# Kernel optimization log

Measured on AMD Instinct MI355X. Metric: run time of the kernel, lower is better.

Reference implementation:

```python
import jax, jax.numpy as jnp
import numpy as np

N = 100000
IN_CH = 256
OUT_CH = 64
HID = 2 * OUT_CH


def _gcn_norm(edge_index, num_nodes):
    # add self-loops, compute symmetric normalization (PyG GCNConv default)
    loop = jnp.arange(num_nodes, dtype=edge_index.dtype)
    row = jnp.concatenate([edge_index[0], loop])  # source
    col = jnp.concatenate([edge_index[1], loop])  # target
    deg = jax.ops.segment_sum(jnp.ones_like(col, dtype=jnp.float32), col,
                              num_segments=num_nodes)
    dinv = jnp.where(deg > 0, jax.lax.rsqrt(deg), 0.0)
    norm = dinv[row] * dinv[col]  # [E+N]
    return row, col, norm


def _gcn_conv(x, W, b, row, col, norm, num_nodes):
    h = x @ W  # [N, F_out] linear first (F_out <= F_in here)
    msg = norm[:, None] * h[row]  # gather + scale, [E+N, F_out]
    out = jax.ops.segment_sum(msg, col, num_segments=num_nodes)
    return out + b


def setup_inputs() -> dict:
    key = jax.random.key(0)
    k1, k2, k3, k4 = jax.random.split(key, 4)
    x = jax.random.normal(k1, (N, IN_CH), dtype=jnp.float32)
    edge_index = jax.random.randint(k2, (2, 1600000), 0, N, dtype=jnp.int64)
    # Glorot-style init like PyG
    W1 = jax.random.normal(k3, (IN_CH, HID), dtype=jnp.float32) / np.sqrt(IN_CH)
    W2 = jax.random.normal(k4, (HID, OUT_CH), dtype=jnp.float32) / np.sqrt(HID)
    b1 = jnp.zeros((HID,), dtype=jnp.float32)
    b2 = jnp.zeros((OUT_CH,), dtype=jnp.float32)
    return {"x": x, "edge_index": edge_index, "W1": W1, "b1": b1, "W2": W2, "b2": b2}


def reference(x, edge_index, W1, b1, W2, b2):
    row, col, norm = _gcn_norm(edge_index, N)
    h = _gcn_conv(x, W1, b1, row, col, norm, N)
    h = jax.nn.relu(h)
    return _gcn_conv(h, W2, b2, row, col, norm, N)
```

## Files before the change

### kernel.cpp

```cpp
#include <hip/hip_runtime.h>
#include <hip/hip_bf16.h>
#include <math.h>

#define IN_CH 256
#define HID 128
#define OUT_CH 64
#define MAXB 128
#define CAP 18432
#define TILE 8192

typedef __attribute__((ext_vector_type(8))) short bf16x8;
typedef __attribute__((ext_vector_type(4))) float f32x4;

__device__ __forceinline__ unsigned int pack_bf2(float a, float b) {
    __hip_bfloat162 h = __float22bfloat162_rn(make_float2(a, b));
    return *(unsigned int*)&h;
}
__device__ __forceinline__ float2 bf2_to_f2(unsigned int v) {
    float2 r;
    r.x = __uint_as_float(v << 16);
    r.y = __uint_as_float(v & 0xffff0000u);
    return r;
}
__device__ __forceinline__ unsigned short f_to_bf1(float f) {
    __hip_bfloat16 h = __float2bfloat16(f);
    return *(unsigned short*)&h;
}
__device__ __forceinline__ void acc8(float4& a, float4& b, uint4 w) {
    float2 p0 = bf2_to_f2(w.x), p1 = bf2_to_f2(w.y);
    float2 p2 = bf2_to_f2(w.z), p3 = bf2_to_f2(w.w);
    a.x += p0.x; a.y += p0.y; a.z += p1.x; a.w += p1.y;
    b.x += p2.x; b.y += p2.y; b.z += p3.x; b.w += p3.y;
}
__device__ __forceinline__ void acc4(float4& a, uint2 w) {
    float2 p0 = bf2_to_f2(w.x), p1 = bf2_to_f2(w.y);
    a.x += p0.x; a.y += p0.y; a.z += p1.x; a.w += p1.y;
}

__global__ void detect_kernel(const void* ei, int E, int N, int* flag) {
    const long long* p = (const long long*)ei;
    int ok = 1;
    for (int j = 0; j < 16; ++j) {
        long long v = p[j];
        if (v < 0 || v >= (long long)N) { ok = 0; break; }
    }
    *flag = ok;
}

__device__ __forceinline__ int edge_at(const void* ei, long long pos, bool is64) {
    return is64 ? (int)((const long long*)ei)[pos] : ((const int*)ei)[pos];
}

__global__ __launch_bounds__(256) void wprep_kernel(const float* __restrict__ W1,
                                                    const float* __restrict__ W2,
                                                    unsigned short* __restrict__ wT1,
                                                    unsigned short* __restrict__ wT2) {
    int t = blockIdx.x * 256 + threadIdx.x;
    if (t < IN_CH * HID) {
        int k = t >> 7, n = t & 127;
        wT1[n * IN_CH + k] = f_to_bf1(W1[t]);
    }
    if (t < HID * OUT_CH) {
        int k = t >> 6, n = t & 63;
        wT2[n * HID + k] = f_to_bf1(W2[t]);
    }
}

__global__ __launch_bounds__(256) void bucket_kernel(const void* ei, int E, int B,
                                                     const int* __restrict__ flag,
                                                     unsigned int* __restrict__ recs,
                                                     int* __restrict__ bcur) {
    __shared__ int cnt[MAXB], off[MAXB], cur[MAXB], gb[MAXB];
    __shared__ unsigned int staged[TILE];
    const bool is64 = (*flag != 0);
    const int t = threadIdx.x;
    const long long base = (long long)blockIdx.x * TILE;

    for (int b = t; b < MAXB; b += 256) cnt[b] = 0;
    __syncthreads();

    for (int i = t; i < TILE; i += 256) {
        long long e = base + i;
        if (e < E) {
            int c = edge_at(ei, (long long)E + e, is64);
            atomicAdd(&cnt[c >> 10], 1);
        }
    }
    __syncthreads();

    if (t < MAXB) off[t] = cnt[t];
    __syncthreads();
    for (int o = 1; o < MAXB; o <<= 1) {
        int v = 0;
        if (t < MAXB && t >= o) v = off[t - o];
        __syncthreads();
        if (t < MAXB) off[t] += v;
        __syncthreads();
    }
    if (t < MAXB) {
        int ex = off[t] - cnt[t];
        off[t] = ex;
        cur[t] = ex;
        gb[t] = 0;
        if (t < B && cnt[t] > 0) gb[t] = atomicAdd(&bcur[t], cnt[t]);
    }
    __syncthreads();

    for (int i = t; i < TILE; i += 256) {
        long long e = base + i;
        if (e < E) {
            int r = edge_at(ei, e, is64);
            int c = edge_at(ei, (long long)E + e, is64);
            int b = c >> 10;
            int p = atomicAdd(&cur[b], 1);
            staged[p] = ((unsigned int)r << 10) | (unsigned int)(c & 1023);
        }
    }
    __syncthreads();

    int wv = t >> 6, ln = t & 63;
    for (int b = wv; b < B; b += 4) {
        int s = off[b];
        int n = cnt[b];
        int gbase = gb[b];
        if (gbase + n > CAP) n = (CAP > gbase) ? (CAP - gbase) : 0;
        for (int j = ln; j < n; j += 64)
            recs[(size_t)b * CAP + gbase + j] = staged[s + j];
    }
}

__global__ __launch_bounds__(512) void csr_kernel(unsigned int* __restrict__ recs,
                                                  const int* __restrict__ bcur,
                                                  int* __restrict__ starts,
                                                  int* __restrict__ cnts,
                                                  float* __restrict__ dinv, int N) {
    __shared__ int degs[1024], lcur[1024], part[512];
    __shared__ unsigned int rows[CAP];
    const int b = blockIdx.x, t = threadIdx.x;
    const int n = min(bcur[b], CAP);
    const size_t rb = (size_t)b * CAP;

    degs[t] = 0;
    degs[t + 512] = 0;
    __syncthreads();
    for (int i = t; i < n; i += 512)
        atomicAdd(&degs[recs[rb + i] & 1023], 1);
    __syncthreads();

    int s0 = degs[2 * t], s1 = degs[2 * t + 1];
    part[t] = s0 + s1;
    __syncthreads();
    for (int o = 1; o < 512; o <<= 1) {
        int v = (t >= o) ? part[t - o] : 0;
        __syncthreads();
        part[t] += v;
        __syncthreads();
    }
    int ex = part[t] - (s0 + s1);
    lcur[2 * t] = ex;
    lcur[2 * t + 1] = ex + s0;

    int node = (b << 10) + 2 * t;
    if (node < N) {
        starts[node] = b * CAP + ex;
        cnts[node] = s0;
        dinv[node] = rsqrtf((float)(s0 + 1));
    }
    if (node + 1 < N) {
        starts[node + 1] = b * CAP + ex + s0;
        cnts[node + 1] = s1;
        dinv[node + 1] = rsqrtf((float)(s1 + 1));
    }
    __syncthreads();

    for (int i = t; i < n; i += 512) {
        unsigned int rc = recs[rb + i];
        int p = atomicAdd(&lcur[rc & 1023], 1);
        rows[p] = rc >> 10;
    }
    __syncthreads();
    for (int i = t; i < n; i += 512) recs[rb + i] = rows[i];
}

__global__ __launch_bounds__(256) void gemm1_kernel(const float* __restrict__ x,
                                                    const unsigned short* __restrict__ wT,
                                                    const float* __restrict__ dinv,
                                                    unsigned short* __restrict__ u, int N) {
    __shared__ uint4 lds4[2048];
    unsigned char* lds = (unsigned char*)lds4;
    const int t = threadIdx.x;
    const int bm0 = blockIdx.x * 128;
    const int wid = t >> 6, lane = t & 63;
    const int l16 = lane & 15, lq = lane >> 4;

    f32x4 acc[2][8];
#pragma unroll
    for (int mf = 0; mf < 2; ++mf)
#pragma unroll
        for (int nf = 0; nf < 8; ++nf) acc[mf][nf] = (f32x4){0.f, 0.f, 0.f, 0.f};

    for (int kc = 0; kc < IN_CH; kc += 64) {
#pragma unroll
        for (int it = 0; it < 4; ++it) {
            int uu = it * 256 + t;
            int r = uu >> 3, c8 = uu & 7;
            int row = bm0 + r;
            float4 v0 = make_float4(0.f, 0.f, 0.f, 0.f), v1 = v0;
            if (row < N) {
                const float* p = &x[(long long)row * IN_CH + kc + c8 * 8];
                v0 = *(const float4*)p;
                v1 = *(const float4*)(p + 4);
            }
            uint4 w;
            w.x = pack_bf2(v0.x, v0.y);
            w.y = pack_bf2(v0.z, v0.w);
            w.z = pack_bf2(v1.x, v1.y);
            w.w = pack_bf2(v1.z, v1.w);
            int off = (r * 128 + c8 * 16) ^ ((r & 7) << 4);
            *(uint4*)&lds[off] = w;
        }
#pragma unroll
        for (int it = 0; it < 4; ++it) {
            int uu = it * 256 + t;
            int n = uu >> 3, c8 = uu & 7;
            uint4 w = *(const uint4*)&wT[n * IN_CH + kc + c8 * 8];
            int off = 16384 + ((n * 128 + c8 * 16) ^ ((n & 7) << 4));
            *(uint4*)&lds[off] = w;
        }
        __syncthreads();
#pragma unroll
        for (int kk = 0; kk < 2; ++kk) {
            int kbyte = kk * 64 + lq * 16;
            bf16x8 a[2], b[8];
#pragma unroll
            for (int mf = 0; mf < 2; ++mf) {
                int r = wid * 32 + mf * 16 + l16;
                int off = (r * 128 + kbyte) ^ ((r & 7) << 4);
                a[mf] = *(const bf16x8*)&lds[off];
            }
#pragma unroll
            for (int nf = 0; nf < 8; ++nf) {
                int n = nf * 16 + l16;
                int off = 16384 + ((n * 128 + kbyte) ^ ((n & 7) << 4));
                b[nf] = *(const bf16x8*)&lds[off];
            }
#pragma unroll
            for (int mf = 0; mf < 2; ++mf)
#pragma unroll
                for (int nf = 0; nf < 8; ++nf)
                    acc[mf][nf] = __builtin_amdgcn_mfma_f32_16x16x32_bf16(
                        a[mf], b[nf], acc[mf][nf], 0, 0, 0);
        }
        __syncthreads();
    }
#pragma unroll
    for (int mf = 0; mf < 2; ++mf) {
#pragma unroll
        for (int j = 0; j < 4; ++j) {
            int row = bm0 + wid * 32 + mf * 16 + lq * 4 + j;
            if (row < N) {
                float dv = dinv[row];
#pragma unroll
                for (int nf = 0; nf < 8; ++nf)
                    u[(long long)row * HID + nf * 16 + l16] = f_to_bf1(acc[mf][nf][j] * dv);
            }
        }
    }
}

__global__ __launch_bounds__(256) void gemm2_kernel(const unsigned short* __restrict__ A,
                                                    const unsigned short* __restrict__ wT,
                                                    const float* __restrict__ dinv,
                                                    unsigned short* __restrict__ u, int N) {
    __shared__ uint4 lds4[1536];
    unsigned char* lds = (unsigned char*)lds4;
    const int t = threadIdx.x;
    const int bm0 = blockIdx.x * 128;
    const int wid = t >> 6, lane = t & 63;
    const int l16 = lane & 15, lq = lane >> 4;

    f32x4 acc[2][4];
#pragma unroll
    for (int mf = 0; mf < 2; ++mf)
#pragma unroll
        for (int nf = 0; nf < 4; ++nf) acc[mf][nf] = (f32x4){0.f, 0.f, 0.f, 0.f};

    for (int kc = 0; kc < HID; kc += 64) {
#pragma unroll
        for (int it = 0; it < 4; ++it) {
            int uu = it * 256 + t;
            int r = uu >> 3, c8 = uu & 7;
            int row = bm0 + r;
            uint4 w = make_uint4(0, 0, 0, 0);
            if (row < N) w = *(const uint4*)&A[(long long)row * HID + kc + c8 * 8];
            int off = (r * 128 + c8 * 16) ^ ((r & 7) << 4);
            *(uint4*)&lds[off] = w;
        }
#pragma unroll
        for (int it = 0; it < 2; ++it) {
            int uu = it * 256 + t;
            int n = uu >> 3, c8 = uu & 7;
            uint4 w = *(const uint4*)&wT[n * HID + kc + c8 * 8];
            int off = 16384 + ((n * 128 + c8 * 16) ^ ((n & 7) << 4));
            *(uint4*)&lds[off] = w;
        }
        __syncthreads();
#pragma unroll
        for (int kk = 0; kk < 2; ++kk) {
            int kbyte = kk * 64 + lq * 16;
            bf16x8 a[2], b[4];
#pragma unroll
            for (int mf = 0; mf < 2; ++mf) {
                int r = wid * 32 + mf * 16 + l16;
                int off = (r * 128 + kbyte) ^ ((r & 7) << 4);
                a[mf] = *(const bf16x8*)&lds[off];
            }
#pragma unroll
            for (int nf = 0; nf < 4; ++nf) {
                int n = nf * 16 + l16;
                int off = 16384 + ((n * 128 + kbyte) ^ ((n & 7) << 4));
                b[nf] = *(const bf16x8*)&lds[off];
            }
#pragma unroll
            for (int mf = 0; mf < 2; ++mf)
#pragma unroll
                for (int nf = 0; nf < 4; ++nf)
                    acc[mf][nf] = __builtin_amdgcn_mfma_f32_16x16x32_bf16(
                        a[mf], b[nf], acc[mf][nf], 0, 0, 0);
        }
        __syncthreads();
    }
#pragma unroll
    for (int mf = 0; mf < 2; ++mf) {
#pragma unroll
        for (int j = 0; j < 4; ++j) {
            int row = bm0 + wid * 32 + mf * 16 + lq * 4 + j;
            if (row < N) {
                float dv = dinv[row];
#pragma unroll
                for (int nf = 0; nf < 4; ++nf)
                    u[(long long)row * OUT_CH + nf * 16 + l16] = f_to_bf1(acc[mf][nf][j] * dv);
            }
        }
    }
}

__global__ __launch_bounds__(256) void agg1_kernel(const uint4* __restrict__ u,
                                                   const int* __restrict__ starts,
                                                   const int* __restrict__ cnts,
                                                   const unsigned int* __restrict__ srow,
                                                   const float* __restrict__ dinv,
                                                   const float* __restrict__ bias,
                                                   unsigned short* __restrict__ out, int N) {
    int wave = threadIdx.x >> 6;
    int lane = threadIdx.x & 63;
    int q = lane >> 4, l16 = lane & 15;
    int node = blockIdx.x * 16 + wave * 4 + q;
    bool act = node < N;
    int nd = act ? node : N - 1;

    float4 sa = make_float4(0.f, 0.f, 0.f, 0.f), sb = sa;
    acc8(sa, sb, u[(size_t)nd * 16 + l16]);

    int beg = starts[nd];
    int cnt = act ? cnts[nd] : 0;
    int j = 0;
    for (; j + 7 < cnt; j += 8) {
        uint4 g[8];
#pragma unroll
        for (int k = 0; k < 8; ++k)
            g[k] = u[(size_t)(int)srow[beg + j + k] * 16 + l16];
#pragma unroll
        for (int k = 0; k < 8; ++k) acc8(sa, sb, g[k]);
    }
    if (j + 3 < cnt) {
        uint4 g[4];
#pragma unroll
        for (int k = 0; k < 4; ++k)
            g[k] = u[(size_t)(int)srow[beg + j + k] * 16 + l16];
#pragma unroll
        for (int k = 0; k < 4; ++k) acc8(sa, sb, g[k]);
        j += 4;
    }
    for (; j < cnt; ++j)
        acc8(sa, sb, u[(size_t)(int)srow[beg + j] * 16 + l16]);

    if (act) {
        float dv = dinv[nd];
        float4 b0 = *(const float4*)&bias[l16 * 8];
        float4 b1v = *(const float4*)&bias[l16 * 8 + 4];
        float o0 = fmaxf(fmaf(dv, sa.x, b0.x), 0.f);
        float o1 = fmaxf(fmaf(dv, sa.y, b0.y), 0.f);
        float o2 = fmaxf(fmaf(dv, sa.z, b0.z), 0.f);
        float o3 = fmaxf(fmaf(dv, sa.w, b0.w), 0.f);
        float o4 = fmaxf(fmaf(dv, sb.x, b1v.x), 0.f);
        float o5 = fmaxf(fmaf(dv, sb.y, b1v.y), 0.f);
        float o6 = fmaxf(fmaf(dv, sb.z, b1v.z), 0.f);
        float o7 = fmaxf(fmaf(dv, sb.w, b1v.w), 0.f);
        uint4 w;
        w.x = pack_bf2(o0, o1);
        w.y = pack_bf2(o2, o3);
        w.z = pack_bf2(o4, o5);
        w.w = pack_bf2(o6, o7);
        *(uint4*)&out[(size_t)node * HID + l16 * 8] = w;
    }
}

__global__ __launch_bounds__(256) void agg2_kernel(const uint2* __restrict__ u,
                                                   const int* __restrict__ starts,
                                                   const int* __restrict__ cnts,
                                                   const unsigned int* __restrict__ srow,
                                                   const float* __restrict__ dinv,
                                                   const float* __restrict__ bias,
                                                   float* __restrict__ out, int N) {
    int wave = threadIdx.x >> 6;
    int lane = threadIdx.x & 63;
    int q = lane >> 4, l16 = lane & 15;
    int node = blockIdx.x * 16 + wave * 4 + q;
    bool act = node < N;
    int nd = act ? node : N - 1;

    float4 s = make_float4(0.f, 0.f, 0.f, 0.f);
    acc4(s, u[(size_t)nd * 16 + l16]);

    int beg = starts[nd];
    int cnt = act ? cnts[nd] : 0;
    int j = 0;
    for (; j + 7 < cnt; j += 8) {
        uint2 g[8];
#pragma unroll
        for (int k = 0; k < 8; ++k)
            g[k] = u[(size_t)(int)srow[beg + j + k] * 16 + l16];
#pragma unroll
        for (int k = 0; k < 8; ++k) acc4(s, g[k]);
    }
    if (j + 3 < cnt) {
        uint2 g[4];
#pragma unroll
        for (int k = 0; k < 4; ++k)
            g[k] = u[(size_t)(int)srow[beg + j + k] * 16 + l16];
#pragma unroll
        for (int k = 0; k < 4; ++k) acc4(s, g[k]);
        j += 4;
    }
    for (; j < cnt; ++j)
        acc4(s, u[(size_t)(int)srow[beg + j] * 16 + l16]);

    if (act) {
        float dv = dinv[nd];
        float4 bb = *(const float4*)&bias[l16 * 4];
        float4 o;
        o.x = fmaf(dv, s.x, bb.x);
        o.y = fmaf(dv, s.y, bb.y);
        o.z = fmaf(dv, s.z, bb.z);
        o.w = fmaf(dv, s.w, bb.w);
        *(float4*)&out[(size_t)node * OUT_CH + l16 * 4] = o;
    }
}

extern "C" void kernel_launch(void* const* d_in, const int* in_sizes, int n_in,
                              void* d_out, int out_size, void* d_ws, size_t ws_size,
                              hipStream_t stream) {
    const float* x  = (const float*)d_in[0];
    const void*  ei = d_in[1];
    const float* W1 = (const float*)d_in[2];
    const float* b1 = (const float*)d_in[3];
    const float* W2 = (const float*)d_in[4];
    const float* b2 = (const float*)d_in[5];
    float* out = (float*)d_out;

    const int N = in_sizes[0] / IN_CH;
    const int E = in_sizes[1] / 2;
    const int B = (N + 1023) >> 10;

    char* ws = (char*)d_ws;
    size_t off = 0;
    auto alloc = [&](size_t bytes) -> void* {
        void* p = ws + off;
        off += (bytes + 255) & ~(size_t)255;
        return p;
    };
    int*            flag   = (int*)alloc(256);
    int*            bcur   = (int*)alloc(MAXB * 4);
    int*            starts = (int*)alloc((size_t)N * 4);
    int*            cnts   = (int*)alloc((size_t)N * 4);
    float*          dinv   = (float*)alloc((size_t)N * 4);
    unsigned int*   recs   = (unsigned int*)alloc((size_t)B * CAP * 4);
    unsigned short* wT1    = (unsigned short*)alloc((size_t)IN_CH * HID * 2);
    unsigned short* wT2    = (unsigned short*)alloc((size_t)HID * OUT_CH * 2);
    unsigned short* u1     = (unsigned short*)alloc((size_t)N * HID * 2);
    unsigned short* hagg   = (unsigned short*)alloc((size_t)N * HID * 2);
    unsigned short* u2     = (unsigned short*)alloc((size_t)N * OUT_CH * 2);

    (void)hipMemsetAsync(bcur, 0, MAXB * 4, stream);
    detect_kernel<<<1, 1, 0, stream>>>(ei, E, N, flag);
    wprep_kernel<<<128, 256, 0, stream>>>(W1, W2, wT1, wT2);
    int tblocks = (E + TILE - 1) / TILE;
    bucket_kernel<<<tblocks, 256, 0, stream>>>(ei, E, B, flag, recs, bcur);
    csr_kernel<<<B, 512, 0, stream>>>(recs, bcur, starts, cnts, dinv, N);

    int gblocks = (N + 127) / 128;
    int ablocks = (N + 15) / 16;
    gemm1_kernel<<<gblocks, 256, 0, stream>>>(x, wT1, dinv, u1, N);
    agg1_kernel<<<ablocks, 256, 0, stream>>>((const uint4*)u1, starts, cnts, recs,
                                             dinv, b1, hagg, N);
    gemm2_kernel<<<gblocks, 256, 0, stream>>>(hagg, wT2, dinv, u2, N);
    agg2_kernel<<<ablocks, 256, 0, stream>>>((const uint2*)u2, starts, cnts, recs,
                                             dinv, b2, out, N);
}
```

Before: 199.7 us.

## Coarsely sort CSR neighbor lists by source block for gather locality

The CSR build now counts edges per (target, source-block) pair, with 16 source ranges of 8192 nodes, in a 64KB shared histogram. It scans that histogram and scatters row ids straight to a new global array, so each node's neighbors are grouped by source range. This replaces the shared-memory staging buffer and copy-back. The aim is better cache locality for the feature gathers in the aggregation kernels, at the cost of more LDS per block, extra serial scan work per thread, and an extra workspace buffer.

```diff
diff --git a/kernel.cpp b/kernel.cpp
--- a/kernel.cpp
+++ b/kernel.cpp
@@ -8,6 +8,8 @@
 #define MAXB 128
 #define CAP 18432
 #define TILE 8192
+#define NBLK 16
+#define SRCSH 13
 
 typedef __attribute__((ext_vector_type(8))) short bf16x8;
 typedef __attribute__((ext_vector_type(4))) float f32x4;
@@ -129,25 +131,33 @@
     }
 }
 
-__global__ __launch_bounds__(512) void csr_kernel(unsigned int* __restrict__ recs,
+__global__ __launch_bounds__(512) void csr_kernel(const unsigned int* __restrict__ recs,
                                                   const int* __restrict__ bcur,
+                                                  unsigned int* __restrict__ srowS,
                                                   int* __restrict__ starts,
                                                   int* __restrict__ cnts,
                                                   float* __restrict__ dinv, int N) {
-    __shared__ int degs[1024], lcur[1024], part[512];
-    __shared__ unsigned int rows[CAP];
+    __shared__ unsigned int cnt2[1024 * NBLK];
+    __shared__ int part[512];
     const int b = blockIdx.x, t = threadIdx.x;
     const int n = min(bcur[b], CAP);
     const size_t rb = (size_t)b * CAP;
 
-    degs[t] = 0;
-    degs[t + 512] = 0;
-    __syncthreads();
-    for (int i = t; i < n; i += 512)
-        atomicAdd(&degs[recs[rb + i] & 1023], 1);
-    __syncthreads();
-
-    int s0 = degs[2 * t], s1 = degs[2 * t + 1];
+    for (int i = t; i < 1024 * NBLK; i += 512) cnt2[i] = 0;
+    __syncthreads();
+
+    for (int i = t; i < n; i += 512) {
+        unsigned int rc = recs[rb + i];
+        atomicAdd(&cnt2[(rc & 1023) * NBLK + (rc >> (10 + SRCSH))], 1u);
+    }
+    __syncthreads();
+
+    const int base_e = t * 32;
+    int s0 = 0, s1 = 0;
+#pragma unroll
+    for (int k = 0; k < NBLK; ++k) s0 += (int)cnt2[base_e + k];
+#pragma unroll
+    for (int k = 0; k < NBLK; ++k) s1 += (int)cnt2[base_e + NBLK + k];
     part[t] = s0 + s1;
     __syncthreads();
     for (int o = 1; o < 512; o <<= 1) {
@@ -157,9 +167,15 @@
         __syncthreads();
     }
     int ex = part[t] - (s0 + s1);
-    lcur[2 * t] = ex;
-    lcur[2 * t + 1] = ex + s0;
-
+    {
+        unsigned int run = (unsigned int)ex;
+#pragma unroll
+        for (int k = 0; k < 32; ++k) {
+            unsigned int c = cnt2[base_e + k];
+            cnt2[base_e + k] = run;
+            run += c;
+        }
+    }
     int node = (b << 10) + 2 * t;
     if (node < N) {
         starts[node] = b * CAP + ex;
@@ -175,11 +191,9 @@
 
     for (int i = t; i < n; i += 512) {
         unsigned int rc = recs[rb + i];
-        int p = atomicAdd(&lcur[rc & 1023], 1);
-        rows[p] = rc >> 10;
-    }
-    __syncthreads();
-    for (int i = t; i < n; i += 512) recs[rb + i] = rows[i];
+        unsigned int p = atomicAdd(&cnt2[(rc & 1023) * NBLK + (rc >> (10 + SRCSH))], 1u);
+        srowS[rb + p] = rc >> 10;
+    }
 }
 
 __global__ __launch_bounds__(256) void gemm1_kernel(const float* __restrict__ x,
@@ -486,6 +500,7 @@
     int*            cnts   = (int*)alloc((size_t)N * 4);
     float*          dinv   = (float*)alloc((size_t)N * 4);
     unsigned int*   recs   = (unsigned int*)alloc((size_t)B * CAP * 4);
+    unsigned int*   srowS  = (unsigned int*)alloc((size_t)B * CAP * 4);
     unsigned short* wT1    = (unsigned short*)alloc((size_t)IN_CH * HID * 2);
     unsigned short* wT2    = (unsigned short*)alloc((size_t)HID * OUT_CH * 2);
     unsigned short* u1     = (unsigned short*)alloc((size_t)N * HID * 2);
@@ -497,14 +512,14 @@
     wprep_kernel<<<128, 256, 0, stream>>>(W1, W2, wT1, wT2);
     int tblocks = (E + TILE - 1) / TILE;
     bucket_kernel<<<tblocks, 256, 0, stream>>>(ei, E, B, flag, recs, bcur);
-    csr_kernel<<<B, 512, 0, stream>>>(recs, bcur, starts, cnts, dinv, N);
+    csr_kernel<<<B, 512, 0, stream>>>(recs, bcur, srowS, starts, cnts, dinv, N);
 
     int gblocks = (N + 127) / 128;
     int ablocks = (N + 15) / 16;
     gemm1_kernel<<<gblocks, 256, 0, stream>>>(x, wT1, dinv, u1, N);
-    agg1_kernel<<<ablocks, 256, 0, stream>>>((const uint4*)u1, starts, cnts, recs,
+    agg1_kernel<<<ablocks, 256, 0, stream>>>((const uint4*)u1, starts, cnts, srowS,
                                              dinv, b1, hagg, N);
     gemm2_kernel<<<gblocks, 256, 0, stream>>>(hagg, wT2, dinv, u2, N);
-    agg2_kernel<<<ablocks, 256, 0, stream>>>((const uint2*)u2, starts, cnts, recs,
+    agg2_kernel<<<ablocks, 256, 0, stream>>>((const uint2*)u2, starts, cnts, srowS,
                                              dinv, b2, out, N);
 }
```

New measurement: 208.4 us. +4.4%, slower.

## Store GEMM outputs in 16-column chunk-major layout and aggregate per chunk

Applied to the files above, without the earlier changes.

GEMM outputs u1, hagg and u2 are now stored in column-chunk-major order ([chunk][node][16] bf16), and the aggregation kernels use a second grid dimension so each block processes a single 16-column chunk. Each feature table slice (N*32 bytes) is small enough to stay cache-resident while edges gather random rows, which should cut the miss traffic from scattered neighbour reads. In exchange, the edge index lists are re-read once per chunk (8x and 4x), each gather moves only 4 bytes per lane, and gemm2 now reads its A operand through strided chunk addressing.

```diff
diff --git a/kernel.cpp b/kernel.cpp
--- a/kernel.cpp
+++ b/kernel.cpp
@@ -25,16 +25,6 @@
 __device__ __forceinline__ unsigned short f_to_bf1(float f) {
     __hip_bfloat16 h = __float2bfloat16(f);
     return *(unsigned short*)&h;
-}
-__device__ __forceinline__ void acc8(float4& a, float4& b, uint4 w) {
-    float2 p0 = bf2_to_f2(w.x), p1 = bf2_to_f2(w.y);
-    float2 p2 = bf2_to_f2(w.z), p3 = bf2_to_f2(w.w);
-    a.x += p0.x; a.y += p0.y; a.z += p1.x; a.w += p1.y;
-    b.x += p2.x; b.y += p2.y; b.z += p3.x; b.w += p3.y;
-}
-__device__ __forceinline__ void acc4(float4& a, uint2 w) {
-    float2 p0 = bf2_to_f2(w.x), p1 = bf2_to_f2(w.y);
-    a.x += p0.x; a.y += p0.y; a.z += p1.x; a.w += p1.y;
 }
 
 __global__ void detect_kernel(const void* ei, int E, int N, int* flag) {
@@ -262,7 +252,7 @@
                 float dv = dinv[row];
 #pragma unroll
                 for (int nf = 0; nf < 8; ++nf)
-                    u[(long long)row * HID + nf * 16 + l16] = f_to_bf1(acc[mf][nf][j] * dv);
+                    u[((size_t)nf * N + row) * 16 + l16] = f_to_bf1(acc[mf][nf][j] * dv);
             }
         }
     }
@@ -292,7 +282,11 @@
             int r = uu >> 3, c8 = uu & 7;
             int row = bm0 + r;
             uint4 w = make_uint4(0, 0, 0, 0);
-            if (row < N) w = *(const uint4*)&A[(long long)row * HID + kc + c8 * 8];
+            if (row < N) {
+                int chunk = (kc >> 4) + (c8 >> 1);
+                const unsigned short* Ac = A + (size_t)chunk * N * 16;
+                w = *(const uint4*)&Ac[(size_t)row * 16 + (c8 & 1) * 8];
+            }
             int off = (r * 128 + c8 * 16) ^ ((r & 7) << 4);
             *(uint4*)&lds[off] = w;
         }
@@ -339,122 +333,126 @@
                 float dv = dinv[row];
 #pragma unroll
                 for (int nf = 0; nf < 4; ++nf)
-                    u[(long long)row * OUT_CH + nf * 16 + l16] = f_to_bf1(acc[mf][nf][j] * dv);
-            }
-        }
-    }
-}
-
-__global__ __launch_bounds__(256) void agg1_kernel(const uint4* __restrict__ u,
+                    u[((size_t)nf * N + row) * 16 + l16] = f_to_bf1(acc[mf][nf][j] * dv);
+            }
+        }
+    }
+}
+
+__global__ __launch_bounds__(256) void agg1_kernel(const unsigned int* __restrict__ u,
                                                    const int* __restrict__ starts,
                                                    const int* __restrict__ cnts,
                                                    const unsigned int* __restrict__ srow,
                                                    const float* __restrict__ dinv,
                                                    const float* __restrict__ bias,
-                                                   unsigned short* __restrict__ out, int N) {
-    int wave = threadIdx.x >> 6;
-    int lane = threadIdx.x & 63;
-    int q = lane >> 4, l16 = lane & 15;
-    int node = blockIdx.x * 16 + wave * 4 + q;
+                                                   unsigned int* __restrict__ out, int N) {
+    const int c = blockIdx.y;
+    const int g = threadIdx.x >> 3, k = threadIdx.x & 7;
+    int node = blockIdx.x * 32 + g;
     bool act = node < N;
     int nd = act ? node : N - 1;
-
-    float4 sa = make_float4(0.f, 0.f, 0.f, 0.f), sb = sa;
-    acc8(sa, sb, u[(size_t)nd * 16 + l16]);
-
+    const unsigned int* tab = u + (size_t)c * N * 8;
+
+    float2 s = bf2_to_f2(tab[(size_t)nd * 8 + k]);
     int beg = starts[nd];
     int cnt = act ? cnts[nd] : 0;
     int j = 0;
     for (; j + 7 < cnt; j += 8) {
-        uint4 g[8];
-#pragma unroll
-        for (int k = 0; k < 8; ++k)
-            g[k] = u[(size_t)(int)srow[beg + j + k] * 16 + l16];
-#pragma unroll
-        for (int k = 0; k < 8; ++k) acc8(sa, sb, g[k]);
+        unsigned int gv[8];
+#pragma unroll
+        for (int q = 0; q < 8; ++q)
+            gv[q] = tab[(size_t)(int)srow[beg + j + q] * 8 + k];
+#pragma unroll
+        for (int q = 0; q < 8; ++q) {
+            float2 v = bf2_to_f2(gv[q]);
+            s.x += v.x;
+            s.y += v.y;
+        }
     }
     if (j + 3 < cnt) {
-        uint4 g[4];
-#pragma unroll
-        for (int k = 0; k < 4; ++k)
-            g[k] = u[(size_t)(int)srow[beg + j + k] * 16 + l16];
-#pragma unroll
-        for (int k = 0; k < 4; ++k) acc8(sa, sb, g[k]);
+        unsigned int gv[4];
+#pragma unroll
+        for (int q = 0; q < 4; ++q)
+            gv[q] = tab[(size_t)(int)srow[beg + j + q] * 8 + k];
+#pragma unroll
+        for (int q = 0; q < 4; ++q) {
+            float2 v = bf2_to_f2(gv[q]);
+            s.x += v.x;
+            s.y += v.y;
+        }
         j += 4;
     }
-    for (; j < cnt; ++j)
-        acc8(sa, sb, u[(size_t)(int)srow[beg + j] * 16 + l16]);
+    for (; j < cnt; ++j) {
+        float2 v = bf2_to_f2(tab[(size_t)(int)srow[beg + j] * 8 + k]);
+        s.x += v.x;
+        s.y += v.y;
+    }
 
     if (act) {
         float dv = dinv[nd];
-        float4 b0 = *(const float4*)&bias[l16 * 8];
-        float4 b1v = *(const float4*)&bias[l16 * 8 + 4];
-        float o0 = fmaxf(fmaf(dv, sa.x, b0.x), 0.f);
-        float o1 = fmaxf(fmaf(dv, sa.y, b0.y), 0.f);
-        float o2 = fmaxf(fmaf(dv, sa.z, b0.z), 0.f);
-        float o3 = fmaxf(fmaf(dv, sa.w, b0.w), 0.f);
-        float o4 = fmaxf(fmaf(dv, sb.x, b1v.x), 0.f);
-        float o5 = fmaxf(fmaf(dv, sb.y, b1v.y), 0.f);
-        float o6 = fmaxf(fmaf(dv, sb.z, b1v.z), 0.f);
-        float o7 = fmaxf(fmaf(dv, sb.w, b1v.w), 0.f);
-        uint4 w;
-        w.x = pack_bf2(o0, o1);
-        w.y = pack_bf2(o2, o3);
-        w.z = pack_bf2(o4, o5);
-        w.w = pack_bf2(o6, o7);
-        *(uint4*)&out[(size_t)node * HID + l16 * 8] = w;
-    }
-}
-
-__global__ __launch_bounds__(256) void agg2_kernel(const uint2* __restrict__ u,
+        float2 bb = *(const float2*)&bias[c * 16 + k * 2];
+        float ox = fmaxf(fmaf(dv, s.x, bb.x), 0.f);
+        float oy = fmaxf(fmaf(dv, s.y, bb.y), 0.f);
+        out[(size_t)c * N * 8 + (size_t)node * 8 + k] = pack_bf2(ox, oy);
+    }
+}
+
+__global__ __launch_bounds__(256) void agg2_kernel(const unsigned int* __restrict__ u,
                                                    const int* __restrict__ starts,
                                                    const int* __restrict__ cnts,
                                                    const unsigned int* __restrict__ srow,
                                                    const float* __restrict__ dinv,
                                                    const float* __restrict__ bias,
                                                    float* __restrict__ out, int N) {
-    int wave = threadIdx.x >> 6;
-    int lane = threadIdx.x & 63;
-    int q = lane >> 4, l16 = lane & 15;
-    int node = blockIdx.x * 16 + wave * 4 + q;
+    const int c = blockIdx.y;
+    const int g = threadIdx.x >> 3, k = threadIdx.x & 7;
+    int node = blockIdx.x * 32 + g;
     bool act = node < N;
     int nd = act ? node : N - 1;
-
-    float4 s = make_float4(0.f, 0.f, 0.f, 0.f);
-    acc4(s, u[(size_t)nd * 16 + l16]);
-
+    const unsigned int* tab = u + (size_t)c * N * 8;
+
+    float2 s = bf2_to_f2(tab[(size_t)nd * 8 + k]);
     int beg = starts[nd];
     int cnt = act ? cnts[nd] : 0;
     int j = 0;
     for (; j + 7 < cnt; j += 8) {
-        uint2 g[8];
-#pragma unroll
-        for (int k = 0; k < 8; ++k)
-            g[k] = u[(size_t)(int)srow[beg + j + k] * 16 + l16];
-#pragma unroll
-        for (int k = 0; k < 8; ++k) acc4(s, g[k]);
+        unsigned int gv[8];
+#pragma unroll
+        for (int q = 0; q < 8; ++q)
+            gv[q] = tab[(size_t)(int)srow[beg + j + q] * 8 + k];
+#pragma unroll
+        for (int q = 0; q < 8; ++q) {
+            float2 v = bf2_to_f2(gv[q]);
+            s.x += v.x;
+            s.y += v.y;
+        }
     }
     if (j + 3 < cnt) {
-        uint2 g[4];
-#pragma unroll
-        for (int k = 0; k < 4; ++k)
-            g[k] = u[(size_t)(int)srow[beg + j + k] * 16 + l16];
-#pragma unroll
-        for (int k = 0; k < 4; ++k) acc4(s, g[k]);
+        unsigned int gv[4];
+#pragma unroll
+        for (int q = 0; q < 4; ++q)
+            gv[q] = tab[(size_t)(int)srow[beg + j + q] * 8 + k];
+#pragma unroll
+        for (int q = 0; q < 4; ++q) {
+            float2 v = bf2_to_f2(gv[q]);
+            s.x += v.x;
+            s.y += v.y;
+        }
         j += 4;
     }
-    for (; j < cnt; ++j)
-        acc4(s, u[(size_t)(int)srow[beg + j] * 16 + l16]);
+    for (; j < cnt; ++j) {
+        float2 v = bf2_to_f2(tab[(size_t)(int)srow[beg + j] * 8 + k]);
+        s.x += v.x;
+        s.y += v.y;
+    }
 
     if (act) {
         float dv = dinv[nd];
-        float4 bb = *(const float4*)&bias[l16 * 4];
-        float4 o;
+        float2 bb = *(const float2*)&bias[c * 16 + k * 2];
+        float2 o;
         o.x = fmaf(dv, s.x, bb.x);
         o.y = fmaf(dv, s.y, bb.y);
-        o.z = fmaf(dv, s.z, bb.z);
-        o.w = fmaf(dv, s.w, bb.w);
-        *(float4*)&out[(size_t)node * OUT_CH + l16 * 4] = o;
+        *(float2*)&out[(size_t)node * OUT_CH + c * 16 + k * 2] = o;
     }
 }
 
@@ -500,11 +498,12 @@
     csr_kernel<<<B, 512, 0, stream>>>(recs, bcur, starts, cnts, dinv, N);
 
     int gblocks = (N + 127) / 128;
-    int ablocks = (N + 15) / 16;
+    int nblocks32 = (N + 31) / 32;
     gemm1_kernel<<<gblocks, 256, 0, stream>>>(x, wT1, dinv, u1, N);
-    agg1_kernel<<<ablocks, 256, 0, stream>>>((const uint4*)u1, starts, cnts, recs,
-                                             dinv, b1, hagg, N);
+    agg1_kernel<<<dim3(nblocks32, 8), 256, 0, stream>>>(
+        (const unsigned int*)u1, starts, cnts, recs, dinv, b1,
+        (unsigned int*)hagg, N);
     gemm2_kernel<<<gblocks, 256, 0, stream>>>(hagg, wT2, dinv, u2, N);
-    agg2_kernel<<<ablocks, 256, 0, stream>>>((const uint2*)u2, starts, cnts, recs,
-                                             dinv, b2, out, N);
-}
+    agg2_kernel<<<dim3(nblocks32, 4), 256, 0, stream>>>(
+        (const unsigned int*)u2, starts, cnts, recs, dinv, b2, out, N);
+}
```

New measurement: 250.6 us. +25.5%, slower.
